# Kernel optimization log

Measured on AMD Instinct MI355X. Metric: run time of the kernel, lower is better.

Reference implementation:

```python
import jax, jax.numpy as jnp
import numpy as np

N, E, B = 10000, 20000, 400
ND, ED, D = 32, 16, 64


def setup_inputs() -> dict:
    key = jax.random.key(0)
    ks = jax.random.split(key, 32)

    def lin(k, out_d, in_d):
        kw, kb = jax.random.split(k)
        s = 1.0 / np.sqrt(in_d)
        return (jax.random.uniform(kw, (out_d, in_d), jnp.float32, -s, s),
                jax.random.uniform(kb, (out_d,), jnp.float32, -s, s))

    W_in, b_in = lin(ks[0], D, ND)
    W_e1, b_e1 = lin(ks[1], D, ED)
    W_e2, b_e2 = lin(ks[2], D * D, D)
    b_conv = jax.random.uniform(ks[3], (D,), jnp.float32, -1/8.0, 1/8.0)
    W_ih, b_ih = lin(ks[4], 3 * D, D)
    W_hh, b_hh = lin(ks[5], 3 * D, D)
    W_ih_l, b_ih_l = lin(ks[6], 4 * D, 2 * D)
    W_hh_l, b_hh_l = lin(ks[7], 4 * D, D)
    W_o1, b_o1 = lin(ks[8], D, 2 * D)
    W_o2, b_o2 = lin(ks[9], 1, D)

    x = jax.random.normal(ks[10], (N, ND), jnp.float32)
    edge_attr = jax.random.normal(ks[11], (E, ED), jnp.float32)
    edge_index = jax.random.randint(ks[12], (2, E), 0, N, jnp.int64)
    batch = jnp.sort(jax.random.randint(ks[13], (N,), 0, B, jnp.int64))

    return dict(x=x, edge_attr=edge_attr,
                W_in=W_in, b_in=b_in, W_e1=W_e1, b_e1=b_e1, W_e2=W_e2, b_e2=b_e2,
                b_conv=b_conv, W_ih=W_ih, b_ih=b_ih, W_hh=W_hh, b_hh=b_hh,
                W_ih_l=W_ih_l, b_ih_l=b_ih_l, W_hh_l=W_hh_l, b_hh_l=b_hh_l,
                W_o1=W_o1, b_o1=b_o1, W_o2=W_o2, b_o2=b_o2,
                edge_index=edge_index, batch=batch)


def reference(x, edge_attr, W_in, b_in, W_e1, b_e1, W_e2, b_e2, b_conv,
              W_ih, b_ih, W_hh, b_hh, W_ih_l, b_ih_l, W_hh_l, b_hh_l,
              W_o1, b_o1, W_o2, b_o2, edge_index, batch):
    src, dst = edge_index[0], edge_index[1]

    # in_linear
    out = jax.nn.relu(x @ W_in.T + b_in)            # [N, D]
    h = out                                          # GRU hidden (layer=1, seq=1)

    # edge-conditioned weights: MLP(edge_attr) -> [E, D, D]
    ew = (jax.nn.relu(edge_attr @ W_e1.T + b_e1) @ W_e2.T + b_e2).reshape(E, D, D)
    cnt = jnp.maximum(jax.ops.segment_sum(jnp.ones((E,), x.dtype), dst, N), 1.0)

    for _ in range(3):
        # NNConv: gather src nodes, per-edge matmul, scatter-mean to dst, + bias
        msg = jnp.einsum('ed,edf->ef', out[src], ew)                 # [E, D]
        agg = jax.ops.segment_sum(msg, dst, N) / cnt[:, None] + b_conv
        m = jax.nn.relu(agg)
        # GRU cell (torch gate order r, z, n)
        gi = m @ W_ih.T + b_ih
        gh = h @ W_hh.T + b_hh
        i_r, i_z, i_n = jnp.split(gi, 3, axis=-1)
        h_r, h_z, h_n = jnp.split(gh, 3, axis=-1)
        r = jax.nn.sigmoid(i_r + h_r)
        z = jax.nn.sigmoid(i_z + h_z)
        n = jnp.tanh(i_n + r * h_n)
        h = (1.0 - z) * n + z * h
        out = h

    # Set2Set pooling, processing_steps=3
    q_star = jnp.zeros((B, 2 * D), x.dtype)
    hl = jnp.zeros((B, D), x.dtype)
    cl = jnp.zeros((B, D), x.dtype)
    for _ in range(3):
        g = q_star @ W_ih_l.T + b_ih_l + hl @ W_hh_l.T + b_hh_l
        gi_, gf_, gg_, go_ = jnp.split(g, 4, axis=-1)   # torch order i,f,g,o
        cl = jax.nn.sigmoid(gf_) * cl + jax.nn.sigmoid(gi_) * jnp.tanh(gg_)
        hl = jax.nn.sigmoid(go_) * jnp.tanh(cl)
        q = hl                                           # [B, D]
        e = jnp.sum(out * q[batch], axis=-1)             # [N]
        mmax = jax.ops.segment_max(e, batch, B)
        a = jnp.exp(e - mmax[batch])
        a = a / jax.ops.segment_sum(a, batch, B)[batch]
        r_ = jax.ops.segment_sum(a[:, None] * out, batch, B)  # [B, D]
        q_star = jnp.concatenate([q, r_], axis=-1)

    o = jax.nn.relu(q_star @ W_o1.T + b_o1) @ W_o2.T + b_o2
    return o.reshape(-1)
```

## Files before the change

kernel.cpp:

```cpp
#include <hip/hip_runtime.h>
#include <math.h>


#define Nn 10000
#define Ee 20000
#define Bb 400
#define KSTEPS 130
#define S2S_CHUNK 1024

typedef __attribute__((ext_vector_type(8))) short bf16x8_t;
typedef __attribute__((ext_vector_type(4))) float f32x4_t;

__device__ __forceinline__ float sigmoidf_(float x) { return 1.f / (1.f + expf(-x)); }

__device__ __forceinline__ void split8(const float* p, bf16x8_t& Ahi_, bf16x8_t& Alo_) {
    union { bf16x8_t v; unsigned u[4]; } hi, lo;
#pragma unroll
    for (int ii = 0; ii < 4; ++ii) {
        float pa = p[2 * ii], pb = p[2 * ii + 1];
        unsigned ua = __float_as_uint(pa), ub = __float_as_uint(pb);
        hi.u[ii] = (ua >> 16) | (ub & 0xFFFF0000u);
        float la = pa - __uint_as_float(ua & 0xFFFF0000u);
        float lb = pb - __uint_as_float(ub & 0xFFFF0000u);
        lo.u[ii] = (__float_as_uint(la) >> 16) | (__float_as_uint(lb) & 0xFFFF0000u);
    }
    Ahi_ = hi.v; Alo_ = lo.v;
}

__global__ __launch_bounds__(256) void k_in_linear(const float* __restrict__ x,
                                                   const float* __restrict__ Win,
                                                   const float* __restrict__ bin,
                                                   float* __restrict__ out) {
    int idx = blockIdx.x * 256 + threadIdx.x;
    if (idx >= Nn * 64) return;
    int n = idx >> 6, j = idx & 63;
    const float* xr = x + n * 32;
    const float* w = Win + j * 32;
    float acc = bin[j];
#pragma unroll
    for (int k = 0; k < 32; ++k) acc += xr[k] * w[k];
    out[idx] = fmaxf(acc, 0.f);
}

__global__ __launch_bounds__(256) void k_edge_mlp1(const float* __restrict__ ea,
                                                   const float* __restrict__ W1,
                                                   const float* __restrict__ b1,
                                                   float* __restrict__ eh) {
    int idx = blockIdx.x * 256 + threadIdx.x;
    if (idx >= Ee * 64) return;
    int e = idx >> 6, j = idx & 63;
    const float* ar = ea + e * 16;
    const float* w = W1 + j * 16;
    float acc = b1[j];
#pragma unroll
    for (int k = 0; k < 16; ++k) acc += ar[k] * w[k];
    eh[idx] = fmaxf(acc, 0.f);
}

__global__ __launch_bounds__(256) void k_make_Bfat(const float* __restrict__ W2,
                                                   const float* __restrict__ b2,
                                                   unsigned short* __restrict__ Bfat) {
    int idx = blockIdx.x * 256 + threadIdx.x;
    if (idx >= KSTEPS * 4096) return;
    int i  = idx & 7;
    int l  = (idx >> 3) & 63;
    int nq = (idx >> 9) & 3;
    int h  = (idx >> 11) & 1;
    int ks = idx >> 12;
    int kap = ks * 32 + (l >> 4) * 8 + i;
    int f = nq * 16 + (l & 15);
    float w;
    if (kap < 4096) {
        int q = kap >> 6, d = kap & 63;
        w = W2[(size_t)(d * 64 + f) * 64 + q];
    } else {
        int d = kap - 4096;
        w = b2[d * 64 + f];
    }
    unsigned u = __float_as_uint(w);
    unsigned short outv;
    if (h == 0) {
        outv = (unsigned short)(u >> 16);
    } else {
        float lo = w - __uint_as_float(u & 0xFFFF0000u);
        outv = (unsigned short)(__float_as_uint(lo) >> 16);
    }
    Bfat[idx] = outv;
}

__global__ __launch_bounds__(256) void k_make_Wg(const float* __restrict__ Wih,
                                                 const float* __restrict__ Whh,
                                                 unsigned short* __restrict__ Wg) {
    int idx = blockIdx.x * 256 + threadIdx.x;
    if (idx >= 4 * 2 * 16 * 64 * 8) return;
    int i  = idx & 7;
    int l  = (idx >> 3) & 63;
    int t  = (idx >> 9) & 15;
    int h  = (idx >> 13) & 1;
    int ks = idx >> 14;
    int k = ks * 32 + (l >> 4) * 8 + i;
    int u = t * 16 + (l & 15);
    int j = u & 63, part = u >> 6;
    float w = 0.f;
    if (part == 0) w = (k < 64) ? Wih[(size_t)j * 64 + k]          : Whh[(size_t)j * 64 + (k - 64)];
    if (part == 1) w = (k < 64) ? Wih[(size_t)(64 + j) * 64 + k]   : Whh[(size_t)(64 + j) * 64 + (k - 64)];
    if (part == 2) w = (k < 64) ? Wih[(size_t)(128 + j) * 64 + k]  : 0.f;
    if (part == 3) w = (k < 64) ? 0.f : Whh[(size_t)(128 + j) * 64 + (k - 64)];
    unsigned uu = __float_as_uint(w);
    unsigned short outv;
    if (h == 0) {
        outv = (unsigned short)(uu >> 16);
    } else {
        float lo = w - __uint_as_float(uu & 0xFFFF0000u);
        outv = (unsigned short)(__float_as_uint(lo) >> 16);
    }
    Wg[idx] = outv;
}

__global__ __launch_bounds__(256, 7) void k_msg_mfma(const float* __restrict__ out,
                                                     const float* __restrict__ eh,
                                                     const unsigned short* __restrict__ Bfat,
                                                     const int* __restrict__ ei,
                                                     float* __restrict__ agg) {
    __shared__ float outs[64][64];
    __shared__ float ehs[64][20];
    int tid = threadIdx.x;
    int ebase = blockIdx.x * 64;
    int ksplit = blockIdx.y;

    int ks0 = ksplit * 32 + (ksplit < 2 ? ksplit : 2);
    int ks1 = ks0 + (ksplit < 2 ? 33 : 32);
    int q0 = ks0 >> 1;
    int qn = ((min(ks1, 128) - 1) >> 1) - q0 + 1;

    {
        int el = tid >> 2, seg = tid & 3;
        int eg = ebase + el;
        bool v = eg < Ee;
        int s = v ? ei[eg] : 0;
        const float* orow = out + (size_t)s * 64 + seg * 16;
        float4 z = make_float4(0.f, 0.f, 0.f, 0.f);
#pragma unroll
        for (int c = 0; c < 4; ++c) {
            float4 ov = v ? *(const float4*)(orow + c * 4) : z;
            int f = (seg * 4 + c) ^ (el & 7);
            *(float4*)&outs[el][f * 4] = ov;
        }
        const float* erow = eh + (size_t)eg * 64;
        for (int j = seg; j < qn; j += 4)
            ehs[el][j] = v ? erow[q0 + j] : 0.f;
    }
    __syncthreads();

    int lane = tid & 63;
    int wtile = tid >> 6;
    int m16 = lane & 15;
    int g = lane >> 4;
    int er = wtile * 16 + m16;
    int esw = er & 7;

    f32x4_t acc[4];
#pragma unroll
    for (int nq = 0; nq < 4; ++nq) acc[nq] = (f32x4_t){0.f, 0.f, 0.f, 0.f};

#pragma unroll 2
    for (int ks = ks0; ks < ks1; ++ks) {
        float ehq = (ks < 128) ? ehs[er][(ks >> 1) - q0] : 1.f;
        int fbase = (ks & 1) * 8 + g * 2;
        float4 o1 = *(const float4*)&outs[er][(fbase ^ esw) * 4];
        float4 o2 = *(const float4*)&outs[er][((fbase + 1) ^ esw) * 4];
        float p[8] = {o1.x * ehq, o1.y * ehq, o1.z * ehq, o1.w * ehq,
                      o2.x * ehq, o2.y * ehq, o2.z * ehq, o2.w * ehq};
        bf16x8_t Ahi, Alo;
        split8(p, Ahi, Alo);
        const unsigned short* bstep = Bfat + (size_t)ks * 4096;
#pragma unroll
        for (int nq = 0; nq < 4; ++nq) {
            bf16x8_t bhi = *(const bf16x8_t*)(bstep + ((size_t)nq * 64 + lane) * 8);
            bf16x8_t blo = *(const bf16x8_t*)(bstep + ((size_t)(4 + nq) * 64 + lane) * 8);
            acc[nq] = __builtin_amdgcn_mfma_f32_16x16x32_bf16(Ahi, bhi, acc[nq], 0, 0, 0);
            acc[nq] = __builtin_amdgcn_mfma_f32_16x16x32_bf16(Ahi, blo, acc[nq], 0, 0, 0);
            acc[nq] = __builtin_amdgcn_mfma_f32_16x16x32_bf16(Alo, bhi, acc[nq], 0, 0, 0);
        }
    }

#pragma unroll
    for (int r = 0; r < 4; ++r) {
        int el = wtile * 16 + g * 4 + r;
        int eg = ebase + el;
        if (eg >= Ee) continue;
        int dn = ei[Ee + eg];
#pragma unroll
        for (int nq = 0; nq < 4; ++nq)
            atomicAdd(&agg[(size_t)dn * 64 + nq * 16 + m16], acc[nq][r]);
    }
}

__global__ __launch_bounds__(256) void k_gru_mfma(const float* __restrict__ agg,
                                                  const float* __restrict__ cnt,
                                                  const float* __restrict__ bconv,
                                                  const unsigned short* __restrict__ Wg,
                                                  const float* __restrict__ bih,
                                                  const float* __restrict__ bhh,
                                                  float* __restrict__ out) {
    __shared__ float ms[64][68];
    __shared__ float hs[64][68];
    int tid = threadIdx.x;
    int nbase = blockIdx.x * 64;

    {
        int nl = tid >> 2, seg = tid & 3;
        int ng = nbase + nl;
        bool v = ng < Nn;
        float c = v ? cnt[ng] : 1.f;
        c = c < 1.f ? 1.f : c;
        float rc = 1.f / c;
        const float* arow = agg + (size_t)ng * 64 + seg * 16;
        const float* hrow = out + (size_t)ng * 64 + seg * 16;
#pragma unroll
        for (int c4 = 0; c4 < 4; ++c4) {
            int col = seg * 16 + c4 * 4;
            float4 z = make_float4(0.f, 0.f, 0.f, 0.f);
            float4 av = v ? *(const float4*)(arow + c4 * 4) : z;
            float4 hv = v ? *(const float4*)(hrow + c4 * 4) : z;
            ms[nl][col + 0] = fmaxf(av.x * rc + bconv[col + 0], 0.f);
            ms[nl][col + 1] = fmaxf(av.y * rc + bconv[col + 1], 0.f);
            ms[nl][col + 2] = fmaxf(av.z * rc + bconv[col + 2], 0.f);
            ms[nl][col + 3] = fmaxf(av.w * rc + bconv[col + 3], 0.f);
            *(float4*)&hs[nl][col] = hv;
        }
    }
    __syncthreads();

    int lane = tid & 63;
    int wtile = tid >> 6;
    int m16 = lane & 15;
    int g = lane >> 4;
    int er = wtile * 16 + m16;

    f32x4_t acc[16];
#pragma unroll
    for (int t = 0; t < 16; ++t) acc[t] = (f32x4_t){0.f, 0.f, 0.f, 0.f};

#pragma unroll
    for (int ks = 0; ks < 4; ++ks) {
        const float* src = (ks < 2) ? &ms[er][ks * 32 + g * 8]
                                    : &hs[er][(ks - 2) * 32 + g * 8];
        float p[8];
#pragma unroll
        for (int ii = 0; ii < 8; ++ii) p[ii] = src[ii];
        bf16x8_t Ahi, Alo;
        split8(p, Ahi, Alo);
        const unsigned short* bstep = Wg + (size_t)ks * (2 * 16 * 512);
#pragma unroll
        for (int t = 0; t < 16; ++t) {
            bf16x8_t bhi = *(const bf16x8_t*)(bstep + ((size_t)t * 64 + lane) * 8);
            bf16x8_t blo = *(const bf16x8_t*)(bstep + ((size_t)(16 + t) * 64 + lane) * 8);
            acc[t] = __builtin_amdgcn_mfma_f32_16x16x32_bf16(Ahi, bhi, acc[t], 0, 0, 0);
            acc[t] = __builtin_amdgcn_mfma_f32_16x16x32_bf16(Ahi, blo, acc[t], 0, 0, 0);
            acc[t] = __builtin_amdgcn_mfma_f32_16x16x32_bf16(Alo, bhi, acc[t], 0, 0, 0);
        }
    }

#pragma unroll
    for (int t2 = 0; t2 < 4; ++t2) {
        int jj = t2 * 16 + m16;
        float br = bih[jj] + bhh[jj];
        float bz = bih[64 + jj] + bhh[64 + jj];
        float bin_ = bih[128 + jj];
        float bhn = bhh[128 + jj];
#pragma unroll
        for (int r = 0; r < 4; ++r) {
            int nl2 = wtile * 16 + g * 4 + r;
            int ng2 = nbase + nl2;
            if (ng2 >= Nn) continue;
            float rg = sigmoidf_(acc[t2][r] + br);
            float z  = sigmoidf_(acc[4 + t2][r] + bz);
            float nn = tanhf(acc[8 + t2][r] + bin_ + rg * (acc[12 + t2][r] + bhn));
            float hv = hs[nl2][jj];
            out[(size_t)ng2 * 64 + jj] = (1.f - z) * nn + z * hv;
        }
    }
}

__global__ __launch_bounds__(256) void k_count_deg(const int* __restrict__ ei,
                                                   float* __restrict__ cnt) {
    int e = blockIdx.x * 256 + threadIdx.x;
    if (e >= Ee) return;
    atomicAdd(&cnt[ei[Ee + e]], 1.f);
}

__global__ __launch_bounds__(256) void k_count_batch(const int* __restrict__ batch,
                                                     int* __restrict__ bcount) {
    int n = blockIdx.x * 256 + threadIdx.x;
    if (n >= Nn) return;
    atomicAdd(&bcount[batch[n]], 1);
}

__global__ __launch_bounds__(64) void k_scan_batch(const int* __restrict__ bcount,
                                                   int* __restrict__ bstart) {
    int lane = threadIdx.x;
    const int PER = (Bb + 63) / 64;
    int base = lane * PER;
    int v[PER];
    int s = 0;
#pragma unroll
    for (int i = 0; i < PER; ++i) {
        int idx = base + i;
        int c = (idx < Bb) ? bcount[idx] : 0;
        v[i] = s;
        s += c;
    }
    int inc = s;
#pragma unroll
    for (int o = 1; o < 64; o <<= 1) {
        int t = __shfl_up(inc, o, 64);
        if (lane >= o) inc += t;
    }
    int excl = inc - s;
    int total = __shfl(inc, 63, 64);
#pragma unroll
    for (int i = 0; i < PER; ++i) {
        int idx = base + i;
        if (idx < Bb) bstart[idx] = excl + v[i];
    }
    if (lane == 63) bstart[Bb] = total;
}

__device__ __forceinline__ float block_reduce_max_(float v, float* red, int tid) {
#pragma unroll
    for (int o = 32; o; o >>= 1) v = fmaxf(v, __shfl_xor(v, o, 64));
    if ((tid & 63) == 0) red[tid >> 6] = v;
    __syncthreads();
    float r = fmaxf(fmaxf(red[0], red[1]), fmaxf(red[2], red[3]));
    __syncthreads();
    return r;
}
__device__ __forceinline__ float block_reduce_sum_(float v, float* red, int tid) {
#pragma unroll
    for (int o = 32; o; o >>= 1) v += __shfl_xor(v, o, 64);
    if ((tid & 63) == 0) red[tid >> 6] = v;
    __syncthreads();
    float r = (red[0] + red[1]) + (red[2] + red[3]);
    __syncthreads();
    return r;
}

__global__ __launch_bounds__(256) void k_set2set(const float* __restrict__ out,
                                                 const int* __restrict__ bstart,
                                                 const float* __restrict__ Wil,
                                                 const float* __restrict__ bil,
                                                 const float* __restrict__ Whl,
                                                 const float* __restrict__ bhl,
                                                 const float* __restrict__ Wo1,
                                                 const float* __restrict__ bo1,
                                                 const float* __restrict__ Wo2,
                                                 const float* __restrict__ bo2,
                                                 float* __restrict__ outp) {
    __shared__ float qs[128];
    __shared__ float hs2[64];
    __shared__ float cs[64];
    __shared__ float g_lds[256];
    __shared__ float e_lds[S2S_CHUNK];
    __shared__ float red[4];
    __shared__ float rpart[4][64];

    int b = blockIdx.x, tid = threadIdx.x;
    int lane = tid & 63, wv = tid >> 6;
    int s = bstart[b], eend = bstart[b + 1];
    int cntb = eend - s;

    if (tid < 128) qs[tid] = 0.f;
    if (tid < 64) { hs2[tid] = 0.f; cs[tid] = 0.f; }
    __syncthreads();

    for (int step = 0; step < 3; ++step) {
        {
            int u = tid;
            float acc = bil[u] + bhl[u];
            const float4* wi = (const float4*)(Wil + (size_t)u * 128);
#pragma unroll
            for (int k4 = 0; k4 < 32; ++k4) {
                float4 w = wi[k4];
                acc += qs[k4 * 4 + 0] * w.x + qs[k4 * 4 + 1] * w.y +
                       qs[k4 * 4 + 2] * w.z + qs[k4 * 4 + 3] * w.w;
            }
            const float4* wh = (const float4*)(Whl + (size_t)u * 64);
#pragma unroll
            for (int k4 = 0; k4 < 16; ++k4) {
                float4 w = wh[k4];
                acc += hs2[k4 * 4 + 0] * w.x + hs2[k4 * 4 + 1] * w.y +
                       hs2[k4 * 4 + 2] * w.z + hs2[k4 * 4 + 3] * w.w;
            }
            g_lds[u] = acc;
        }
        __syncthreads();
        if (tid < 64) {
            float c = sigmoidf_(g_lds[64 + tid]) * cs[tid] +
                      sigmoidf_(g_lds[tid]) * tanhf(g_lds[128 + tid]);
            cs[tid] = c;
            float h = sigmoidf_(g_lds[192 + tid]) * tanhf(c);
            hs2[tid] = h;
            qs[tid] = h;
        }
        __syncthreads();

        float gmax = -INFINITY, gsum = 0.f, racc = 0.f;
        for (int c0 = s; c0 < eend; c0 += S2S_CHUNK) {
            int clen = min(S2S_CHUNK, eend - c0);
            for (int i = tid; i < clen; i += 256) {
                const float4* orow = (const float4*)(out + (size_t)(c0 + i) * 64);
                float a0 = 0.f, a1 = 0.f, a2 = 0.f, a3 = 0.f;
#pragma unroll
                for (int k4 = 0; k4 < 16; k4 += 4) {
                    float4 o0 = orow[k4], o1 = orow[k4 + 1], o2 = orow[k4 + 2], o3 = orow[k4 + 3];
                    a0 += o0.x * qs[k4 * 4 + 0]  + o0.y * qs[k4 * 4 + 1]  + o0.z * qs[k4 * 4 + 2]  + o0.w * qs[k4 * 4 + 3];
                    a1 += o1.x * qs[k4 * 4 + 4]  + o1.y * qs[k4 * 4 + 5]  + o1.z * qs[k4 * 4 + 6]  + o1.w * qs[k4 * 4 + 7];
                    a2 += o2.x * qs[k4 * 4 + 8]  + o2.y * qs[k4 * 4 + 9]  + o2.z * qs[k4 * 4 + 10] + o2.w * qs[k4 * 4 + 11];
                    a3 += o3.x * qs[k4 * 4 + 12] + o3.y * qs[k4 * 4 + 13] + o3.z * qs[k4 * 4 + 14] + o3.w * qs[k4 * 4 + 15];
                }
                e_lds[i] = (a0 + a1) + (a2 + a3);
            }
            __syncthreads();
            float m = -INFINITY;
            for (int i = tid; i < clen; i += 256) m = fmaxf(m, e_lds[i]);
            float cmax = block_reduce_max_(m, red, tid);
            float nm = fmaxf(gmax, cmax);
            float scale = expf(gmax - nm);
            gsum *= scale; racc *= scale;
            float lsum = 0.f;
            for (int i = tid; i < clen; i += 256) {
                float av = expf(e_lds[i] - nm);
                e_lds[i] = av;
                lsum += av;
            }
            gsum += block_reduce_sum_(lsum, red, tid);
            for (int i = wv; i < clen; i += 4)
                racc += e_lds[i] * out[(size_t)(c0 + i) * 64 + lane];
            gmax = nm;
            __syncthreads();
        }
        rpart[wv][lane] = racc;
        __syncthreads();
        if (tid < 64) {
            float r = (rpart[0][tid] + rpart[1][tid]) + (rpart[2][tid] + rpart[3][tid]);
            qs[64 + tid] = (cntb > 0) ? r / gsum : 0.f;
        }
        __syncthreads();
    }

    if (tid < 64) {
        float acc = bo1[tid];
        const float4* w = (const float4*)(Wo1 + (size_t)tid * 128);
#pragma unroll
        for (int k4 = 0; k4 < 32; ++k4) {
            float4 wv4 = w[k4];
            acc += qs[k4 * 4 + 0] * wv4.x + qs[k4 * 4 + 1] * wv4.y +
                   qs[k4 * 4 + 2] * wv4.z + qs[k4 * 4 + 3] * wv4.w;
        }
        acc = fmaxf(acc, 0.f);
        float t = acc * Wo2[tid];
#pragma unroll
        for (int o = 32; o; o >>= 1) t += __shfl_xor(t, o, 64);
        if (tid == 0) outp[b] = t + bo2[0];
    }
}

extern "C" void kernel_launch(void* const* d_in, const int* in_sizes, int n_in,
                              void* d_out, int out_size, void* d_ws, size_t ws_size,
                              hipStream_t stream) {
    const float* x        = (const float*)d_in[0];
    const float* ea       = (const float*)d_in[1];
    const float* W_in     = (const float*)d_in[2];
    const float* b_in     = (const float*)d_in[3];
    const float* W_e1     = (const float*)d_in[4];
    const float* b_e1     = (const float*)d_in[5];
    const float* W_e2     = (const float*)d_in[6];
    const float* b_e2     = (const float*)d_in[7];
    const float* b_conv   = (const float*)d_in[8];
    const float* W_ih     = (const float*)d_in[9];
    const float* b_ih     = (const float*)d_in[10];
    const float* W_hh     = (const float*)d_in[11];
    const float* b_hh     = (const float*)d_in[12];
    const float* W_ih_l   = (const float*)d_in[13];
    const float* b_ih_l   = (const float*)d_in[14];
    const float* W_hh_l   = (const float*)d_in[15];
    const float* b_hh_l   = (const float*)d_in[16];
    const float* W_o1     = (const float*)d_in[17];
    const float* b_o1     = (const float*)d_in[18];
    const float* W_o2     = (const float*)d_in[19];
    const float* b_o2     = (const float*)d_in[20];
    const int*   ei       = (const int*)d_in[21];
    const int*   batch    = (const int*)d_in[22];
    float* outp = (float*)d_out;

    char* base = (char*)d_ws;
    size_t off = 0;
    auto carve = [&](size_t bytes) -> void* {
        void* p = base + off;
        off = (off + bytes + 255) & ~(size_t)255;
        return p;
    };
    float* out    = (float*)carve((size_t)Nn * 64 * 4);
    float* agg    = (float*)carve((size_t)Nn * 64 * 4);
    float* eh     = (float*)carve((size_t)Ee * 64 * 4);
    unsigned short* Bfat = (unsigned short*)carve((size_t)KSTEPS * 4096 * 2);
    unsigned short* Wg   = (unsigned short*)carve((size_t)4 * 2 * 16 * 64 * 8 * 2);
    float* cnt    = (float*)carve((size_t)Nn * 4);
    int*   bcount = (int*)carve((size_t)Bb * 4);
    int*   bstart = (int*)carve((size_t)(Bb + 1) * 4);
    if (off > ws_size) return;

    hipMemsetAsync(cnt, 0, (size_t)Nn * 4, stream);
    hipMemsetAsync(bcount, 0, (size_t)Bb * 4, stream);

    k_in_linear<<<(Nn * 64) / 256, 256, 0, stream>>>(x, W_in, b_in, out);
    k_edge_mlp1<<<(Ee * 64) / 256, 256, 0, stream>>>(ea, W_e1, b_e1, eh);
    k_make_Bfat<<<(KSTEPS * 4096) / 256, 256, 0, stream>>>(W_e2, b_e2, Bfat);
    k_make_Wg<<<(4 * 2 * 16 * 64 * 8) / 256, 256, 0, stream>>>(W_ih, W_hh, Wg);
    k_count_deg<<<(Ee + 255) / 256, 256, 0, stream>>>(ei, cnt);
    k_count_batch<<<(Nn + 255) / 256, 256, 0, stream>>>(batch, bcount);
    k_scan_batch<<<1, 64, 0, stream>>>(bcount, bstart);

    int eblocks = (Ee + 63) / 64;
    int nblocks = (Nn + 63) / 64;
    for (int it = 0; it < 3; ++it) {
        hipMemsetAsync(agg, 0, (size_t)Nn * 64 * 4, stream);
        k_msg_mfma<<<dim3(eblocks, 4), 256, 0, stream>>>(out, eh, Bfat, ei, agg);
        k_gru_mfma<<<nblocks, 256, 0, stream>>>(agg, cnt, b_conv, Wg, b_ih, b_hh, out);
    }

    k_set2set<<<Bb, 256, 0, stream>>>(out, bstart, W_ih_l, b_ih_l, W_hh_l, b_hh_l,
                                      W_o1, b_o1, W_o2, b_o2, outp);
}
```

Before: 386.2 us.

## Sort edges by destination into CSR and aggregate messages per node without atomics

Builds a CSR layout (degree count, scan, counting sort) so edges are grouped by destination node, and permutes edge hidden features into that order. The message kernel now processes 64-node blocks, walking each block's edges in tiles, reducing per-node sums in shared memory, and writing one partial sum per k-split into a separate buffer that the GRU kernel adds up. This removes the float atomics and the per-iteration memset of agg. In exchange it adds extra syncs and a serial row reduction, and blocks whose nodes have many edges take longer, which unbalances the work. The k-split count also rises from 4 to 8.

Result: slower. 592.1 us (+53.3%).

```diff
diff --git a/kernel.cpp b/kernel.cpp
--- a/kernel.cpp
+++ b/kernel.cpp
@@ -45,6 +45,7 @@
 __global__ __launch_bounds__(256) void k_edge_mlp1(const float* __restrict__ ea,
                                                    const float* __restrict__ W1,
                                                    const float* __restrict__ b1,
+                                                   const int* __restrict__ epos,
                                                    float* __restrict__ eh) {
     int idx = blockIdx.x * 256 + threadIdx.x;
     if (idx >= Ee * 64) return;
@@ -54,7 +55,7 @@
     float acc = b1[j];
 #pragma unroll
     for (int k = 0; k < 16; ++k) acc += ar[k] * w[k];
-    eh[idx] = fmaxf(acc, 0.f);
+    eh[(size_t)epos[e] * 64 + j] = fmaxf(acc, 0.f);
 }
 
 __global__ __launch_bounds__(256) void k_make_Bfat(const float* __restrict__ W2,
@@ -117,40 +118,76 @@
     Wg[idx] = outv;
 }
 
-__global__ __launch_bounds__(256, 7) void k_msg_mfma(const float* __restrict__ out,
-                                                     const float* __restrict__ eh,
-                                                     const unsigned short* __restrict__ Bfat,
-                                                     const int* __restrict__ ei,
-                                                     float* __restrict__ agg) {
+__global__ __launch_bounds__(256) void k_count_deg(const int* __restrict__ ei,
+                                                   int* __restrict__ deg) {
+    int e = blockIdx.x * 256 + threadIdx.x;
+    if (e >= Ee) return;
+    atomicAdd(&deg[ei[Ee + e]], 1);
+}
+
+__global__ __launch_bounds__(256) void k_scan_nodes(const int* __restrict__ deg,
+                                                    int* __restrict__ rowptr,
+                                                    int* __restrict__ wptr) {
+    __shared__ int part[256];
+    int t = threadIdx.x;
+    const int PER = (Nn + 255) / 256;
+    int b0 = t * PER;
+    int s = 0;
+    for (int i = 0; i < PER; ++i) {
+        int idx = b0 + i;
+        if (idx < Nn) s += deg[idx];
+    }
+    part[t] = s;
+    __syncthreads();
+    for (int o = 1; o < 256; o <<= 1) {
+        int u = (t >= o) ? part[t - o] : 0;
+        __syncthreads();
+        part[t] += u;
+        __syncthreads();
+    }
+    int run = part[t] - s;
+    for (int i = 0; i < PER; ++i) {
+        int idx = b0 + i;
+        if (idx < Nn) {
+            rowptr[idx] = run;
+            wptr[idx] = run;
+            run += deg[idx];
+        }
+    }
+    if (t == 255) rowptr[Nn] = run;
+}
+
+__global__ __launch_bounds__(256) void k_sort_edges(const int* __restrict__ ei,
+                                                    int* __restrict__ wptr,
+                                                    int* __restrict__ srcs,
+                                                    int* __restrict__ epos) {
+    int e = blockIdx.x * 256 + threadIdx.x;
+    if (e >= Ee) return;
+    int d = ei[Ee + e];
+    int p = atomicAdd(&wptr[d], 1);
+    srcs[p] = ei[e];
+    epos[e] = p;
+}
+
+__global__ __launch_bounds__(256, 5) void k_msg_nodes(const float* __restrict__ out,
+                                                      const float* __restrict__ eh,
+                                                      const unsigned short* __restrict__ Bfat,
+                                                      const int* __restrict__ srcs,
+                                                      const int* __restrict__ rowptr,
+                                                      float* __restrict__ agg4,
+                                                      int nsplit) {
     __shared__ float outs[64][64];
-    __shared__ float ehs[64][20];
+    __shared__ float ehs_t[64][64];
     int tid = threadIdx.x;
-    int ebase = blockIdx.x * 64;
+    int nbase = blockIdx.x * 64;
     int ksplit = blockIdx.y;
-
-    int ks0 = ksplit * 32 + (ksplit < 2 ? ksplit : 2);
-    int ks1 = ks0 + (ksplit < 2 ? 33 : 32);
-    int q0 = ks0 >> 1;
-    int qn = ((min(ks1, 128) - 1) >> 1) - q0 + 1;
-
-    {
-        int el = tid >> 2, seg = tid & 3;
-        int eg = ebase + el;
-        bool v = eg < Ee;
-        int s = v ? ei[eg] : 0;
-        const float* orow = out + (size_t)s * 64 + seg * 16;
-        float4 z = make_float4(0.f, 0.f, 0.f, 0.f);
-#pragma unroll
-        for (int c = 0; c < 4; ++c) {
-            float4 ov = v ? *(const float4*)(orow + c * 4) : z;
-            int f = (seg * 4 + c) ^ (el & 7);
-            *(float4*)&outs[el][f * 4] = ov;
-        }
-        const float* erow = eh + (size_t)eg * 64;
-        for (int j = seg; j < qn; j += 4)
-            ehs[el][j] = v ? erow[q0 + j] : 0.f;
-    }
-    __syncthreads();
+    int ks0 = (KSTEPS * ksplit) / nsplit;
+    int ks1 = (KSTEPS * (ksplit + 1)) / nsplit;
+
+    int rs = rowptr[nbase];
+    int re = rowptr[min(nbase + 64, Nn)];
+    int ecount = re - rs;
+    int ntiles = (ecount + 63) >> 6;
 
     int lane = tid & 63;
     int wtile = tid >> 6;
@@ -159,50 +196,109 @@
     int er = wtile * 16 + m16;
     int esw = er & 7;
 
-    f32x4_t acc[4];
-#pragma unroll
-    for (int nq = 0; nq < 4; ++nq) acc[nq] = (f32x4_t){0.f, 0.f, 0.f, 0.f};
-
-#pragma unroll 2
-    for (int ks = ks0; ks < ks1; ++ks) {
-        float ehq = (ks < 128) ? ehs[er][(ks >> 1) - q0] : 1.f;
-        int fbase = (ks & 1) * 8 + g * 2;
-        float4 o1 = *(const float4*)&outs[er][(fbase ^ esw) * 4];
-        float4 o2 = *(const float4*)&outs[er][((fbase + 1) ^ esw) * 4];
-        float p[8] = {o1.x * ehq, o1.y * ehq, o1.z * ehq, o1.w * ehq,
-                      o2.x * ehq, o2.y * ehq, o2.z * ehq, o2.w * ehq};
-        bf16x8_t Ahi, Alo;
-        split8(p, Ahi, Alo);
-        const unsigned short* bstep = Bfat + (size_t)ks * 4096;
-#pragma unroll
-        for (int nq = 0; nq < 4; ++nq) {
-            bf16x8_t bhi = *(const bf16x8_t*)(bstep + ((size_t)nq * 64 + lane) * 8);
-            bf16x8_t blo = *(const bf16x8_t*)(bstep + ((size_t)(4 + nq) * 64 + lane) * 8);
-            acc[nq] = __builtin_amdgcn_mfma_f32_16x16x32_bf16(Ahi, bhi, acc[nq], 0, 0, 0);
-            acc[nq] = __builtin_amdgcn_mfma_f32_16x16x32_bf16(Ahi, blo, acc[nq], 0, 0, 0);
-            acc[nq] = __builtin_amdgcn_mfma_f32_16x16x32_bf16(Alo, bhi, acc[nq], 0, 0, 0);
-        }
-    }
-
-#pragma unroll
-    for (int r = 0; r < 4; ++r) {
-        int el = wtile * 16 + g * 4 + r;
-        int eg = ebase + el;
-        if (eg >= Ee) continue;
-        int dn = ei[Ee + eg];
+    int nl = tid >> 2;
+    int cs = (tid & 3) * 16;
+    int ng = nbase + nl;
+    int gs = (ng < Nn) ? rowptr[ng] - rs : 0;
+    int ge = (ng < Nn) ? rowptr[ng + 1] - rs : 0;
+    float racc[16];
+#pragma unroll
+    for (int i = 0; i < 16; ++i) racc[i] = 0.f;
+
+    for (int tile = 0; tile < ntiles; ++tile) {
+        int tstart = tile << 6;
+        {
+            int el = tid >> 2, seg = tid & 3;
+            int i = tstart + el;
+            bool v = i < ecount;
+            int ir = v ? rs + i : 0;
+            int sN = srcs[ir];
+            const float* orow = out + (size_t)sN * 64 + seg * 16;
+            const float* erow = eh + (size_t)ir * 64 + seg * 16;
+            float4 z = make_float4(0.f, 0.f, 0.f, 0.f);
+#pragma unroll
+            for (int c = 0; c < 4; ++c) {
+                float4 ov = v ? *(const float4*)(orow + c * 4) : z;
+                int f = (seg * 4 + c) ^ (el & 7);
+                *(float4*)&outs[el][f * 4] = ov;
+                float4 ev = v ? *(const float4*)(erow + c * 4) : z;
+                int q = seg * 16 + c * 4;
+                ehs_t[q + 0][el] = ev.x;
+                ehs_t[q + 1][el] = ev.y;
+                ehs_t[q + 2][el] = ev.z;
+                ehs_t[q + 3][el] = ev.w;
+            }
+        }
+        __syncthreads();
+
+        f32x4_t acc[4];
+#pragma unroll
+        for (int nq = 0; nq < 4; ++nq) acc[nq] = (f32x4_t){0.f, 0.f, 0.f, 0.f};
+
+        for (int ks = ks0; ks < ks1; ++ks) {
+            float ehq; int fbase;
+            if (ks < 128) { ehq = ehs_t[ks >> 1][er]; fbase = (ks & 1) * 8 + g * 2; }
+            else          { ehq = 1.f;               fbase = (ks - 128) * 8 + g * 2; }
+            float4 o1 = *(const float4*)&outs[er][(fbase ^ esw) * 4];
+            float4 o2 = *(const float4*)&outs[er][((fbase + 1) ^ esw) * 4];
+            float p[8] = {o1.x * ehq, o1.y * ehq, o1.z * ehq, o1.w * ehq,
+                          o2.x * ehq, o2.y * ehq, o2.z * ehq, o2.w * ehq};
+            bf16x8_t Ahi, Alo;
+            split8(p, Ahi, Alo);
+            const unsigned short* bstep = Bfat + (size_t)ks * 4096;
+#pragma unroll
+            for (int nq = 0; nq < 4; ++nq) {
+                bf16x8_t bhi = *(const bf16x8_t*)(bstep + ((size_t)nq * 64 + lane) * 8);
+                bf16x8_t blo = *(const bf16x8_t*)(bstep + ((size_t)(4 + nq) * 64 + lane) * 8);
+                acc[nq] = __builtin_amdgcn_mfma_f32_16x16x32_bf16(Ahi, bhi, acc[nq], 0, 0, 0);
+                acc[nq] = __builtin_amdgcn_mfma_f32_16x16x32_bf16(Ahi, blo, acc[nq], 0, 0, 0);
+                acc[nq] = __builtin_amdgcn_mfma_f32_16x16x32_bf16(Alo, bhi, acc[nq], 0, 0, 0);
+            }
+        }
+        __syncthreads();
+
 #pragma unroll
         for (int nq = 0; nq < 4; ++nq)
-            atomicAdd(&agg[(size_t)dn * 64 + nq * 16 + m16], acc[nq][r]);
-    }
-}
-
-__global__ __launch_bounds__(256) void k_gru_mfma(const float* __restrict__ agg,
-                                                  const float* __restrict__ cnt,
+#pragma unroll
+            for (int r = 0; r < 4; ++r)
+                outs[wtile * 16 + g * 4 + r][nq * 16 + m16] = acc[nq][r];
+        __syncthreads();
+
+        int il = gs - tstart; if (il < 0) il = 0;
+        int tcap = ecount - tstart; if (tcap > 64) tcap = 64;
+        int ih = ge - tstart; if (ih > tcap) ih = tcap;
+        for (int r = il; r < ih; ++r) {
+#pragma unroll
+            for (int c = 0; c < 4; ++c) {
+                float4 mv = *(const float4*)&outs[r][cs + c * 4];
+                racc[c * 4 + 0] += mv.x;
+                racc[c * 4 + 1] += mv.y;
+                racc[c * 4 + 2] += mv.z;
+                racc[c * 4 + 3] += mv.w;
+            }
+        }
+        __syncthreads();
+    }
+
+    if (ng < Nn) {
+        float* arow = agg4 + ((size_t)ksplit * Nn + ng) * 64 + cs;
+#pragma unroll
+        for (int c = 0; c < 4; ++c) {
+            float4 sv = make_float4(racc[c * 4 + 0], racc[c * 4 + 1],
+                                    racc[c * 4 + 2], racc[c * 4 + 3]);
+            *(float4*)(arow + c * 4) = sv;
+        }
+    }
+}
+
+__global__ __launch_bounds__(256) void k_gru_mfma(const float* __restrict__ agg4,
+                                                  const int* __restrict__ rowptr,
                                                   const float* __restrict__ bconv,
                                                   const unsigned short* __restrict__ Wg,
                                                   const float* __restrict__ bih,
                                                   const float* __restrict__ bhh,
-                                                  float* __restrict__ out) {
+                                                  float* __restrict__ out,
+                                                  int nsplit) {
     __shared__ float ms[64][68];
     __shared__ float hs[64][68];
     int tid = threadIdx.x;
@@ -212,16 +308,19 @@
         int nl = tid >> 2, seg = tid & 3;
         int ng = nbase + nl;
         bool v = ng < Nn;
-        float c = v ? cnt[ng] : 1.f;
-        c = c < 1.f ? 1.f : c;
-        float rc = 1.f / c;
-        const float* arow = agg + (size_t)ng * 64 + seg * 16;
+        int dg = v ? rowptr[ng + 1] - rowptr[ng] : 1;
+        if (dg < 1) dg = 1;
+        float rc = 1.f / (float)dg;
         const float* hrow = out + (size_t)ng * 64 + seg * 16;
 #pragma unroll
         for (int c4 = 0; c4 < 4; ++c4) {
             int col = seg * 16 + c4 * 4;
             float4 z = make_float4(0.f, 0.f, 0.f, 0.f);
-            float4 av = v ? *(const float4*)(arow + c4 * 4) : z;
+            float4 av = z;
+            for (int sp = 0; sp < nsplit; ++sp) {
+                float4 t = v ? *(const float4*)(agg4 + ((size_t)sp * Nn + ng) * 64 + col) : z;
+                av.x += t.x; av.y += t.y; av.z += t.z; av.w += t.w;
+            }
             float4 hv = v ? *(const float4*)(hrow + c4 * 4) : z;
             ms[nl][col + 0] = fmaxf(av.x * rc + bconv[col + 0], 0.f);
             ms[nl][col + 1] = fmaxf(av.y * rc + bconv[col + 1], 0.f);
@@ -281,13 +380,6 @@
             out[(size_t)ng2 * 64 + jj] = (1.f - z) * nn + z * hv;
         }
     }
-}
-
-__global__ __launch_bounds__(256) void k_count_deg(const int* __restrict__ ei,
-                                                   float* __restrict__ cnt) {
-    int e = blockIdx.x * 256 + threadIdx.x;
-    if (e >= Ee) return;
-    atomicAdd(&cnt[ei[Ee + e]], 1.f);
 }
 
 __global__ __launch_bounds__(256) void k_count_batch(const int* __restrict__ batch,
@@ -501,33 +593,47 @@
         off = (off + bytes + 255) & ~(size_t)255;
         return p;
     };
-    float* out    = (float*)carve((size_t)Nn * 64 * 4);
-    float* agg    = (float*)carve((size_t)Nn * 64 * 4);
-    float* eh     = (float*)carve((size_t)Ee * 64 * 4);
-    unsigned short* Bfat = (unsigned short*)carve((size_t)KSTEPS * 4096 * 2);
-    unsigned short* Wg   = (unsigned short*)carve((size_t)4 * 2 * 16 * 64 * 8 * 2);
-    float* cnt    = (float*)carve((size_t)Nn * 4);
-    int*   bcount = (int*)carve((size_t)Bb * 4);
-    int*   bstart = (int*)carve((size_t)(Bb + 1) * 4);
+
+    int ns = 8;
+    float *out, *agg4, *eh;
+    unsigned short *Bfat, *Wg;
+    int *srcs, *epos, *rowptr, *wptr, *deg, *bcount, *bstart;
+    for (;; ns >>= 1) {
+        off = 0;
+        out    = (float*)carve((size_t)Nn * 64 * 4);
+        agg4   = (float*)carve((size_t)ns * Nn * 64 * 4);
+        eh     = (float*)carve((size_t)Ee * 64 * 4);
+        Bfat   = (unsigned short*)carve((size_t)KSTEPS * 4096 * 2);
+        Wg     = (unsigned short*)carve((size_t)4 * 2 * 16 * 64 * 8 * 2);
+        srcs   = (int*)carve((size_t)Ee * 4);
+        epos   = (int*)carve((size_t)Ee * 4);
+        rowptr = (int*)carve((size_t)(Nn + 1) * 4);
+        wptr   = (int*)carve((size_t)Nn * 4);
+        deg    = (int*)carve((size_t)Nn * 4);
+        bcount = (int*)carve((size_t)Bb * 4);
+        bstart = (int*)carve((size_t)(Bb + 1) * 4);
+        if (off <= ws_size || ns == 1) break;
+    }
     if (off > ws_size) return;
 
-    hipMemsetAsync(cnt, 0, (size_t)Nn * 4, stream);
+    hipMemsetAsync(deg, 0, (size_t)Nn * 4, stream);
     hipMemsetAsync(bcount, 0, (size_t)Bb * 4, stream);
 
+    k_count_deg<<<(Ee + 255) / 256, 256, 0, stream>>>(ei, deg);
+    k_scan_nodes<<<1, 256, 0, stream>>>(deg, rowptr, wptr);
+    k_sort_edges<<<(Ee + 255) / 256, 256, 0, stream>>>(ei, wptr, srcs, epos);
+
     k_in_linear<<<(Nn * 64) / 256, 256, 0, stream>>>(x, W_in, b_in, out);
-    k_edge_mlp1<<<(Ee * 64) / 256, 256, 0, stream>>>(ea, W_e1, b_e1, eh);
+    k_edge_mlp1<<<(Ee * 64) / 256, 256, 0, stream>>>(ea, W_e1, b_e1, epos, eh);
     k_make_Bfat<<<(KSTEPS * 4096) / 256, 256, 0, stream>>>(W_e2, b_e2, Bfat);
     k_make_Wg<<<(4 * 2 * 16 * 64 * 8) / 256, 256, 0, stream>>>(W_ih, W_hh, Wg);
-    k_count_deg<<<(Ee + 255) / 256, 256, 0, stream>>>(ei, cnt);
     k_count_batch<<<(Nn + 255) / 256, 256, 0, stream>>>(batch, bcount);
     k_scan_batch<<<1, 64, 0, stream>>>(bcount, bstart);
 
-    int eblocks = (Ee + 63) / 64;
     int nblocks = (Nn + 63) / 64;
     for (int it = 0; it < 3; ++it) {
-        hipMemsetAsync(agg, 0, (size_t)Nn * 64 * 4, stream);
-        k_msg_mfma<<<dim3(eblocks, 4), 256, 0, stream>>>(out, eh, Bfat, ei, agg);
-        k_gru_mfma<<<nblocks, 256, 0, stream>>>(agg, cnt, b_conv, Wg, b_ih, b_hh, out);
+        k_msg_nodes<<<dim3(nblocks, ns), 256, 0, stream>>>(out, eh, Bfat, srcs, rowptr, agg4, ns);
+        k_gru_mfma<<<nblocks, 256, 0, stream>>>(agg4, rowptr, b_conv, Wg, b_ih, b_hh, out, ns);
     }
 
     k_set2set<<<Bb, 256, 0, stream>>>(out, bstart, W_ih_l, b_ih_l, W_hh_l, b_hh_l,
```

## Stage edge-weight B tiles in LDS and process two edge tiles per wave

Applied to the files above, without the earlier changes.

The message kernel now handles 128 edges per block instead of 64. Each wave computes two 16-row edge tiles that share the same B fragments. Each k-step's B tile is copied into shared memory, with the next step's tile prefetched into registers while the current one is used, instead of every wave reading B straight from global memory. This halves B traffic per edge and hides load latency, at the cost of two block barriers per k-step, more shared memory, a lower occupancy target and half as many blocks.

Measured after the change: 335.9 us. 1.15x faster.

```diff
diff --git a/kernel.cpp b/kernel.cpp
--- a/kernel.cpp
+++ b/kernel.cpp
@@ -117,15 +117,16 @@
     Wg[idx] = outv;
 }
 
-__global__ __launch_bounds__(256, 7) void k_msg_mfma(const float* __restrict__ out,
+__global__ __launch_bounds__(256, 3) void k_msg_mfma(const float* __restrict__ out,
                                                      const float* __restrict__ eh,
                                                      const unsigned short* __restrict__ Bfat,
                                                      const int* __restrict__ ei,
                                                      float* __restrict__ agg) {
-    __shared__ float outs[64][64];
-    __shared__ float ehs[64][20];
+    __shared__ float outs[128][64];
+    __shared__ float ehs[128][20];
+    __shared__ unsigned short Bst[4096];
     int tid = threadIdx.x;
-    int ebase = blockIdx.x * 64;
+    int ebase = blockIdx.x * 128;
     int ksplit = blockIdx.y;
 
     int ks0 = ksplit * 32 + (ksplit < 2 ? ksplit : 2);
@@ -133,8 +134,9 @@
     int q0 = ks0 >> 1;
     int qn = ((min(ks1, 128) - 1) >> 1) - q0 + 1;
 
-    {
-        int el = tid >> 2, seg = tid & 3;
+#pragma unroll
+    for (int pass = 0; pass < 2; ++pass) {
+        int el = pass * 64 + (tid >> 2), seg = tid & 3;
         int eg = ebase + el;
         bool v = eg < Ee;
         int s = v ? ei[eg] : 0;
@@ -150,49 +152,91 @@
         for (int j = seg; j < qn; j += 4)
             ehs[el][j] = v ? erow[q0 + j] : 0.f;
     }
-    __syncthreads();
+
+    const float4* bsrc = (const float4*)(Bfat + (size_t)ks0 * 4096);
+    float4 bpre0 = bsrc[tid];
+    float4 bpre1 = bsrc[256 + tid];
 
     int lane = tid & 63;
     int wtile = tid >> 6;
     int m16 = lane & 15;
     int g = lane >> 4;
-    int er = wtile * 16 + m16;
-    int esw = er & 7;
-
-    f32x4_t acc[4];
-#pragma unroll
-    for (int nq = 0; nq < 4; ++nq) acc[nq] = (f32x4_t){0.f, 0.f, 0.f, 0.f};
-
-#pragma unroll 2
+    int erA = wtile * 32 + m16;
+    int erB = erA + 16;
+    int eswA = erA & 7;
+    int eswB = erB & 7;
+
+    f32x4_t acc[2][4];
+#pragma unroll
+    for (int t = 0; t < 2; ++t)
+#pragma unroll
+        for (int nq = 0; nq < 4; ++nq) acc[t][nq] = (f32x4_t){0.f, 0.f, 0.f, 0.f};
+
     for (int ks = ks0; ks < ks1; ++ks) {
-        float ehq = (ks < 128) ? ehs[er][(ks >> 1) - q0] : 1.f;
-        int fbase = (ks & 1) * 8 + g * 2;
-        float4 o1 = *(const float4*)&outs[er][(fbase ^ esw) * 4];
-        float4 o2 = *(const float4*)&outs[er][((fbase + 1) ^ esw) * 4];
-        float p[8] = {o1.x * ehq, o1.y * ehq, o1.z * ehq, o1.w * ehq,
-                      o2.x * ehq, o2.y * ehq, o2.z * ehq, o2.w * ehq};
-        bf16x8_t Ahi, Alo;
-        split8(p, Ahi, Alo);
-        const unsigned short* bstep = Bfat + (size_t)ks * 4096;
+        *(float4*)&Bst[(size_t)tid * 8] = bpre0;
+        *(float4*)&Bst[2048 + (size_t)tid * 8] = bpre1;
+        __syncthreads();
+
+        if (ks + 1 < ks1) {
+            const float4* bn = (const float4*)(Bfat + (size_t)(ks + 1) * 4096);
+            bpre0 = bn[tid];
+            bpre1 = bn[256 + tid];
+        }
+
+        bf16x8_t bhi[4], blo[4];
 #pragma unroll
         for (int nq = 0; nq < 4; ++nq) {
-            bf16x8_t bhi = *(const bf16x8_t*)(bstep + ((size_t)nq * 64 + lane) * 8);
-            bf16x8_t blo = *(const bf16x8_t*)(bstep + ((size_t)(4 + nq) * 64 + lane) * 8);
-            acc[nq] = __builtin_amdgcn_mfma_f32_16x16x32_bf16(Ahi, bhi, acc[nq], 0, 0, 0);
-            acc[nq] = __builtin_amdgcn_mfma_f32_16x16x32_bf16(Ahi, blo, acc[nq], 0, 0, 0);
-            acc[nq] = __builtin_amdgcn_mfma_f32_16x16x32_bf16(Alo, bhi, acc[nq], 0, 0, 0);
-        }
-    }
-
-#pragma unroll
-    for (int r = 0; r < 4; ++r) {
-        int el = wtile * 16 + g * 4 + r;
-        int eg = ebase + el;
-        if (eg >= Ee) continue;
-        int dn = ei[Ee + eg];
-#pragma unroll
-        for (int nq = 0; nq < 4; ++nq)
-            atomicAdd(&agg[(size_t)dn * 64 + nq * 16 + m16], acc[nq][r]);
+            bhi[nq] = *(const bf16x8_t*)&Bst[((size_t)nq * 64 + lane) * 8];
+            blo[nq] = *(const bf16x8_t*)&Bst[((size_t)(4 + nq) * 64 + lane) * 8];
+        }
+
+        int fbase = (ks < 128) ? (ks & 1) * 8 + g * 2 : (ks - 128) * 8 + g * 2;
+
+        {
+            float ehq = (ks < 128) ? ehs[erA][(ks >> 1) - q0] : 1.f;
+            float4 o1 = *(const float4*)&outs[erA][(fbase ^ eswA) * 4];
+            float4 o2 = *(const float4*)&outs[erA][((fbase + 1) ^ eswA) * 4];
+            float p[8] = {o1.x * ehq, o1.y * ehq, o1.z * ehq, o1.w * ehq,
+                          o2.x * ehq, o2.y * ehq, o2.z * ehq, o2.w * ehq};
+            bf16x8_t Ahi, Alo;
+            split8(p, Ahi, Alo);
+#pragma unroll
+            for (int nq = 0; nq < 4; ++nq) {
+                acc[0][nq] = __builtin_amdgcn_mfma_f32_16x16x32_bf16(Ahi, bhi[nq], acc[0][nq], 0, 0, 0);
+                acc[0][nq] = __builtin_amdgcn_mfma_f32_16x16x32_bf16(Ahi, blo[nq], acc[0][nq], 0, 0, 0);
+                acc[0][nq] = __builtin_amdgcn_mfma_f32_16x16x32_bf16(Alo, bhi[nq], acc[0][nq], 0, 0, 0);
+            }
+        }
+        {
+            float ehq = (ks < 128) ? ehs[erB][(ks >> 1) - q0] : 1.f;
+            float4 o1 = *(const float4*)&outs[erB][(fbase ^ eswB) * 4];
+            float4 o2 = *(const float4*)&outs[erB][((fbase + 1) ^ eswB) * 4];
+            float p[8] = {o1.x * ehq, o1.y * ehq, o1.z * ehq, o1.w * ehq,
+                          o2.x * ehq, o2.y * ehq, o2.z * ehq, o2.w * ehq};
+            bf16x8_t Ahi, Alo;
+            split8(p, Ahi, Alo);
+#pragma unroll
+            for (int nq = 0; nq < 4; ++nq) {
+                acc[1][nq] = __builtin_amdgcn_mfma_f32_16x16x32_bf16(Ahi, bhi[nq], acc[1][nq], 0, 0, 0);
+                acc[1][nq] = __builtin_amdgcn_mfma_f32_16x16x32_bf16(Ahi, blo[nq], acc[1][nq], 0, 0, 0);
+                acc[1][nq] = __builtin_amdgcn_mfma_f32_16x16x32_bf16(Alo, bhi[nq], acc[1][nq], 0, 0, 0);
+            }
+        }
+        __syncthreads();
+    }
+
+#pragma unroll
+    for (int t = 0; t < 2; ++t) {
+#pragma unroll
+        for (int r = 0; r < 4; ++r) {
+            int el = wtile * 32 + t * 16 + g * 4 + r;
+            int eg = ebase + el;
+            if (eg >= Ee) continue;
+            int dn = ei[Ee + eg];
+#pragma unroll
+            for (int nq = 0; nq < 4; ++nq)
+                atomicAdd(&agg[(size_t)dn * 64 + nq * 16 + m16], acc[t][nq][r]);
+        }
     }
 }
 
@@ -522,7 +566,7 @@
     k_count_batch<<<(Nn + 255) / 256, 256, 0, stream>>>(batch, bcount);
     k_scan_batch<<<1, 64, 0, stream>>>(bcount, bstart);
 
-    int eblocks = (Ee + 63) / 64;
+    int eblocks = (Ee + 127) / 128;
     int nblocks = (Nn + 63) / 64;
     for (int it = 0; it < 3; ++it) {
         hipMemsetAsync(agg, 0, (size_t)Nn * 64 * 4, stream);
```
